# Kernel optimization log

Hardware: AMD Instinct MI355X
Metric: run time of the kernel (lower is better)

## Reference

```python
import jax, jax.numpy as jnp
import numpy as np

EPS = 1e-10      # normalizer eps from the torch module
IN_EPS = 1e-5    # torch InstanceNorm2d default eps
STRIDE = 2
PAD = 1


def _dw_conv_transpose(x, W):
    """Depthwise ConvTranspose2d applied for every output channel at once.

    x: [B, Cin, H, W]
    W: [Cin, Cout, kh, kw]  (W[:, i] is sub_convs[i].weight of shape [Cin, 1, kh, kw])
    returns: [B, Cin, Cout, H', W'] where channel (c, i) = convT of x[:, c] with W[c, i].
    """
    Cin, Cout, kh, kw = W.shape
    # Transposed conv == dilated conv with spatially flipped kernel,
    # lhs_dilation = stride, padding = k - 1 - pad (output_padding = 0).
    rhs = jnp.flip(W, axis=(-2, -1)).reshape(Cin * Cout, 1, kh, kw)
    pad_h = (kh - 1 - PAD, kh - 1 - PAD)
    pad_w = (kw - 1 - PAD, kw - 1 - PAD)
    out = jax.lax.conv_general_dilated(
        x, rhs,
        window_strides=(1, 1),
        padding=(pad_h, pad_w),
        lhs_dilation=(STRIDE, STRIDE),
        dimension_numbers=('NCHW', 'OIHW', 'NCHW'),
        feature_group_count=Cin,
    )  # [B, Cin*Cout, H', W'], group-major: group c -> channels c*Cout:(c+1)*Cout
    B = x.shape[0]
    return out.reshape(B, Cin, Cout, out.shape[2], out.shape[3])


def setup_inputs() -> dict:
    key = jax.random.key(0)
    k1, k2, k3 = jax.random.split(key, 3)
    B, Cin, Cout, H, Wd, K = 2, 64, 64, 48, 48, 4
    x = jax.random.normal(k1, (B, Cin, H, Wd), dtype=jnp.float32)
    # Positive-leaning weights keep the normalizer (convT of ones) away from zero.
    W = 0.05 + 0.1 * jax.random.uniform(k2, (Cin, Cout, K, K), dtype=jnp.float32)
    bias = 0.02 * jax.random.normal(k3, (Cout,), dtype=jnp.float32)
    return {"x": x, "W": W, "bias": bias}


def reference(x, W, bias):
    # numerator: depthwise convT of the input for every (in_ch, out_ch) pair
    num = _dw_conv_transpose(x, W)                       # [B, Cin, Cout, H', W']
    # normalizer: same convT applied to ones (batch-independent -> batch of 1)
    den = _dw_conv_transpose(jnp.ones_like(x[:1]), W) + EPS  # [1, Cin, Cout, H', W']
    out = jnp.sum(num / den, axis=1) + bias[None, :, None, None]  # [B, Cout, H', W']
    # InstanceNorm2d (no affine, biased variance) over spatial dims per (b, c)
    mean = jnp.mean(out, axis=(2, 3), keepdims=True)
    var = jnp.var(out, axis=(2, 3), keepdims=True)
    return (out - mean) / jnp.sqrt(var + IN_EPS)
```

## Files before the change

### kernel.cpp

```cpp
#include <hip/hip_runtime.h>

#define BB    2
#define CIN   64
#define NI    64
#define HIN   48
#define WIN   48
#define HO    96
#define WO    96
#define EPSN  1e-10f
#define IN_EPS 1e-5f
#define IMG   (HO*WO)
#define NIMG  (BB*NI)
#define PH    50
#define PW    52
#define XPN   (BB*CIN*PH*PW)

__global__ __launch_bounds__(256) void pad_kernel(const float* __restrict__ x,
                                                  float* __restrict__ xpad) {
    const int slice = blockIdx.x >> 1, half = blockIdx.x & 1;
    const float* xs = x + (size_t)slice * (HIN * WIN);
    float* xd = xpad + (size_t)slice * (PH * PW) + half * 25 * PW;
    for (int e = threadIdx.x; e < 25 * PW; e += 256) {
        const int rp = e / PW, pc = e - rp * PW;
        const int h = half * 25 + rp - 1, w = pc - 1;
        float v = 0.f;
        if ((unsigned)h < HIN && (unsigned)w < WIN) v = xs[h * WIN + w];
        xd[e] = v;
    }
}

template <int CS>
__global__ __launch_bounds__(256) void conv_kernel(
        const float* __restrict__ xpad, const float* __restrict__ Wt,
        float* __restrict__ part) {
    constexpr int NC = CIN / CS;
    const int bi = blockIdx.x, s = blockIdx.y;
    const int b = bi >> 6, i = bi & 63, c0 = s * NC;
    const int tid = threadIdx.x;
    const int ty = tid >> 4, tx = tid & 15;

    __shared__ __align__(16) float sF[NC * 16];
    __shared__ float sW[NC * 16];
    __shared__ float sR[NC * 16];
    __shared__ float sFix[384];

    for (int e = tid; e < NC * 16; e += 256) {
        const int c = e >> 4, j = e & 15;
        const float* wp = Wt + ((size_t)(c0 + c) * NI + i) * 16;
        sW[e] = wp[j];
        const int py = (j >> 3) & 1, px = (j >> 2) & 1, a = (j >> 1) & 1, bb = j & 1;
        const int kh = py ? (a ? 2 : 0) : (a ? 3 : 1);
        const int kw = px ? (bb ? 2 : 0) : (bb ? 3 : 1);
        const int r0 = py ? 0 : 1, r1 = py ? 2 : 3;
        const int q0 = px ? 0 : 1, q1 = px ? 2 : 3;
        const float den = wp[r0 * 4 + q0] + wp[r0 * 4 + q1]
                        + wp[r1 * 4 + q0] + wp[r1 * 4 + q1];
        sF[e] = wp[kh * 4 + kw] / (den + EPSN);
        const int cy = j >> 2, cx = j & 3;
        const int THn[4] = {1, 2, 2, 1};
        const int THv[4][2] = {{1, 1}, {0, 2}, {1, 3}, {2, 2}};
        float den2 = 0.f;
        for (int aa = 0; aa < THn[cy]; ++aa)
            for (int bb2 = 0; bb2 < THn[cx]; ++bb2)
                den2 += wp[THv[cy][aa] * 4 + THv[cx][bb2]];
        sR[e] = 1.f / (den2 + EPSN);
    }
    __syncthreads();

    float acc[6][6];
#pragma unroll
    for (int r = 0; r < 6; ++r)
#pragma unroll
        for (int j = 0; j < 6; ++j) acc[r][j] = 0.f;

    const float* xb = xpad + ((size_t)b * CIN + c0) * (PH * PW) + (3 * ty) * PW + 3 * tx;

#pragma unroll 2
    for (int c = 0; c < NC; ++c) {
        float g[16];
        const float4* gf = (const float4*)&sF[c * 16];
#pragma unroll
        for (int q = 0; q < 4; ++q) {
            const float4 t = gf[q];
            g[4 * q] = t.x; g[4 * q + 1] = t.y; g[4 * q + 2] = t.z; g[4 * q + 3] = t.w;
        }

        const float* xc = xb + c * (PH * PW);
        float xv[5][5];
#pragma unroll
        for (int rr = 0; rr < 5; ++rr)
#pragma unroll
            for (int cc = 0; cc < 5; ++cc) xv[rr][cc] = xc[rr * PW + cc];

#pragma unroll
        for (int r = 0; r < 6; ++r) {
            const int rhi = (r + 3) >> 1, rlo = rhi - 1, py = r & 1;
#pragma unroll
            for (int j = 0; j < 6; ++j) {
                const int chi = (j + 3) >> 1, clo = chi - 1, px = j & 1;
                const float* gg = &g[py * 8 + px * 4];
                acc[r][j] += xv[rhi][chi] * gg[0] + xv[rhi][clo] * gg[1]
                           + xv[rlo][chi] * gg[2] + xv[rlo][clo] * gg[3];
            }
        }
    }

    const float* xb2 = xpad + ((size_t)b * CIN + c0) * (PH * PW);
    for (int p = tid; p < 380; p += 256) {
        int y, xo;
        if (p < 96)       { y = 0;            xo = p; }
        else if (p < 192) { y = 95;           xo = p - 96; }
        else if (p < 286) { y = p - 192 + 1;  xo = 0; }
        else              { y = p - 286 + 1;  xo = 95; }
        const int hA = (y + 1) >> 1, hB = hA - 1;
        const int khA = (y & 1) ? 0 : 1, khB = khA + 2;
        const int wA = (xo + 1) >> 1, wB = wA - 1;
        const int kwA = (xo & 1) ? 0 : 1, kwB = kwA + 2;
        const int cy = (y == 0) ? 0 : (y == 95) ? 3 : ((y & 1) ? 1 : 2);
        const int cx = (xo == 0) ? 0 : (xo == 95) ? 3 : ((xo & 1) ? 1 : 2);
        const int cls = cy * 4 + cx;
        const int rA = (hA + 1) * PW, rB = (hB + 1) * PW;
        float v = 0.f;
        for (int c = 0; c < NC; ++c) {
            const float* xc = xb2 + c * (PH * PW);
            const float* wc = &sW[c * 16];
            const float num = xc[rA + wA + 1] * wc[khA * 4 + kwA]
                            + xc[rA + wB + 1] * wc[khA * 4 + kwB]
                            + xc[rB + wA + 1] * wc[khB * 4 + kwA]
                            + xc[rB + wB + 1] * wc[khB * 4 + kwB];
            v += num * sR[c * 16 + cls];
        }
        sFix[p] = v;
    }
    __syncthreads();

#pragma unroll
    for (int r = 0; r < 6; ++r)
#pragma unroll
        for (int j = 0; j < 6; ++j) {
            const int y = 6 * ty + r, xo = 6 * tx + j;
            if (y == 0)        acc[r][j] = sFix[xo];
            else if (y == 95)  acc[r][j] = sFix[96 + xo];
            else if (xo == 0)  acc[r][j] = sFix[192 + y - 1];
            else if (xo == 95) acc[r][j] = sFix[286 + y - 1];
        }

    float* pp = part + ((size_t)s * NIMG + bi) * IMG + (6 * ty) * WO + 6 * tx;
#pragma unroll
    for (int r = 0; r < 6; ++r)
#pragma unroll
        for (int jj = 0; jj < 3; ++jj) {
            float2 v;
            v.x = acc[r][2 * jj];
            v.y = acc[r][2 * jj + 1];
            *(float2*)(pp + r * WO + 2 * jj) = v;
        }
}

template <int CS>
__global__ __launch_bounds__(768) void epilogue_kernel(
        const float* __restrict__ part, const float* __restrict__ bias,
        float* __restrict__ out) {
    const int bi = blockIdx.x;
    const int tid = threadIdx.x;
    const float bv = bias[bi & 63];
    const float4* pb = (const float4*)part + (size_t)bi * (IMG / 4);
    const size_t stride4 = (size_t)NIMG * (IMG / 4);

    float4 v[3];
    float s1 = 0.f, s2 = 0.f;
#pragma unroll
    for (int k = 0; k < 3; ++k) {
        const int idx = k * 768 + tid;
        float4 t = pb[idx];
#pragma unroll
        for (int s = 1; s < CS; ++s) {
            const float4 q = pb[s * stride4 + idx];
            t.x += q.x; t.y += q.y; t.z += q.z; t.w += q.w;
        }
        t.x += bv; t.y += bv; t.z += bv; t.w += bv;
        v[k] = t;
        s1 += t.x + t.y + t.z + t.w;
        s2 += t.x * t.x + t.y * t.y + t.z * t.z + t.w * t.w;
    }

    __shared__ float red[24];
    __shared__ float stat[2];
#pragma unroll
    for (int off = 32; off > 0; off >>= 1) {
        s1 += __shfl_down(s1, off, 64);
        s2 += __shfl_down(s2, off, 64);
    }
    const int w = tid >> 6;
    if ((tid & 63) == 0) { red[w] = s1; red[12 + w] = s2; }
    __syncthreads();
    if (tid == 0) {
        float t1 = 0.f, t2 = 0.f;
#pragma unroll
        for (int k = 0; k < 12; ++k) { t1 += red[k]; t2 += red[12 + k]; }
        const float mean = t1 * (1.f / 9216.f);
        const float m2 = t2 * (1.f / 9216.f);
        stat[0] = mean;
        stat[1] = rsqrtf(m2 - mean * mean + IN_EPS);
    }
    __syncthreads();
    const float mean = stat[0], inv = stat[1];

    float4* ob = (float4*)out + (size_t)bi * (IMG / 4);
#pragma unroll
    for (int k = 0; k < 3; ++k) {
        const int idx = k * 768 + tid;
        float4 t = v[k];
        t.x = (t.x - mean) * inv; t.y = (t.y - mean) * inv;
        t.z = (t.z - mean) * inv; t.w = (t.w - mean) * inv;
        ob[idx] = t;
    }
}

extern "C" void kernel_launch(void* const* d_in, const int* in_sizes, int n_in,
                              void* d_out, int out_size, void* d_ws, size_t ws_size,
                              hipStream_t stream) {
    const float* x    = (const float*)d_in[0];
    const float* Wt   = (const float*)d_in[1];
    const float* bias = (const float*)d_in[2];
    float* out = (float*)d_out;
    float* ws  = (float*)d_ws;

    float* xpad = ws;
    pad_kernel<<<BB * CIN * 2, 256, 0, stream>>>(x, xpad);

    const size_t need4 = ((size_t)XPN + (size_t)4 * NIMG * IMG) * 4;
    if (ws_size >= need4) {
        float* part = ws + XPN;
        conv_kernel<4><<<dim3(NIMG, 4), 256, 0, stream>>>(xpad, Wt, part);
        epilogue_kernel<4><<<NIMG, 768, 0, stream>>>(part, bias, out);
    } else {
        conv_kernel<1><<<dim3(NIMG, 1), 256, 0, stream>>>(xpad, Wt, out);
        epilogue_kernel<1><<<NIMG, 768, 0, stream>>>(out, bias, out);
    }
}
```

Before: 96.68 us.

## Recast depthwise convT sum as fp16 MFMA GEMM over channels

Replaces the FP32 scalar conv with a channel-last fp16 layout of x and precomputed fp16 normalized weight matrices, so the per-phase 2x2 taps become MFMA 16x16x32 GEMMs reducing over input channels. The split-channel partial buffers and their summation go away, and border pixels are fixed up in the epilogue instead of the conv. The intent is to move the dominant FLOPs onto matrix cores and cut partial-sum traffic. In exchange it adds fp16 rounding of inputs and weights, and it uses static device globals instead of the workspace.

```diff
diff --git a/kernel.cpp b/kernel.cpp
--- a/kernel.cpp
+++ b/kernel.cpp
@@ -11,172 +11,200 @@
 #define IN_EPS 1e-5f
 #define IMG   (HO*WO)
 #define NIMG  (BB*NI)
-#define PH    50
-#define PW    52
-#define XPN   (BB*CIN*PH*PW)
-
-__global__ __launch_bounds__(256) void pad_kernel(const float* __restrict__ x,
-                                                  float* __restrict__ xpad) {
-    const int slice = blockIdx.x >> 1, half = blockIdx.x & 1;
-    const float* xs = x + (size_t)slice * (HIN * WIN);
-    float* xd = xpad + (size_t)slice * (PH * PW) + half * 25 * PW;
-    for (int e = threadIdx.x; e < 25 * PW; e += 256) {
-        const int rp = e / PW, pc = e - rp * PW;
-        const int h = half * 25 + rp - 1, w = pc - 1;
-        float v = 0.f;
-        if ((unsigned)h < HIN && (unsigned)w < WIN) v = xs[h * WIN + w];
-        xd[e] = v;
-    }
-}
-
-template <int CS>
-__global__ __launch_bounds__(256) void conv_kernel(
-        const float* __restrict__ xpad, const float* __restrict__ Wt,
-        float* __restrict__ part) {
-    constexpr int NC = CIN / CS;
-    const int bi = blockIdx.x, s = blockIdx.y;
-    const int b = bi >> 6, i = bi & 63, c0 = s * NC;
+
+#define XTROW 50
+#define XTSL  (XTROW*XTROW*64)
+
+using half8  = __attribute__((ext_vector_type(8))) _Float16;
+using half2v = __attribute__((ext_vector_type(2))) _Float16;
+using f32x4  = __attribute__((ext_vector_type(4))) float;
+
+__device__ _Float16 g_xt[BB * XTSL];
+__device__ _Float16 g_G[16 * 64 * 64];
+__device__ float    g_out[NIMG * IMG];
+
+__global__ __launch_bounds__(256) void prep_kernel(const float* __restrict__ x,
+                                                   const float* __restrict__ Wt) {
+    const int blk = blockIdx.x;
     const int tid = threadIdx.x;
-    const int ty = tid >> 4, tx = tid & 15;
-
-    __shared__ __align__(16) float sF[NC * 16];
-    __shared__ float sW[NC * 16];
-    __shared__ float sR[NC * 16];
+
+    if (blk < 96) {
+        const int b = blk / 48, h = blk - 48 * b, hp = h + 1;
+        __shared__ float sT[64][49];
+        for (int e = tid; e < 64 * 12; e += 256) {
+            const int c = e / 12, w4 = e - 12 * c;
+            const float4 t = *(const float4*)(x + ((size_t)(b * 64 + c) * 48 + h) * 48 + 4 * w4);
+            sT[c][4 * w4]     = t.x;
+            sT[c][4 * w4 + 1] = t.y;
+            sT[c][4 * w4 + 2] = t.z;
+            sT[c][4 * w4 + 3] = t.w;
+        }
+        __syncthreads();
+        _Float16* xr = g_xt + (size_t)b * XTSL + (size_t)hp * (XTROW * 64);
+        for (int e = tid; e < XTROW * 32; e += 256) {
+            const int wp = e >> 5, cp = e & 31;
+            half2v hv;
+            if (wp == 0 || wp == 49) { hv[0] = (_Float16)0.f; hv[1] = (_Float16)0.f; }
+            else { hv[0] = (_Float16)sT[2 * cp][wp - 1]; hv[1] = (_Float16)sT[2 * cp + 1][wp - 1]; }
+            *(half2v*)(xr + wp * 64 + 2 * cp) = hv;
+        }
+        return;
+    }
+    if (blk < 100) {
+        const int z = blk - 96;
+        const int b = z >> 1, hp = (z & 1) ? 49 : 0;
+        _Float16* xr = g_xt + (size_t)b * XTSL + (size_t)hp * (XTROW * 64);
+        half2v hz; hz[0] = (_Float16)0.f; hz[1] = (_Float16)0.f;
+        for (int e = tid; e < XTROW * 32; e += 256)
+            *(half2v*)(xr + (e >> 5) * 64 + 2 * (e & 31)) = hz;
+        return;
+    }
+    const int combo = blk - 100;
+    const int py = combo >> 3, px = (combo >> 2) & 1, a = (combo >> 1) & 1, bb = combo & 1;
+    const int kh = 2 * a + 1 - py, kw = 2 * bb + 1 - px;
+    for (int e = tid; e < 4096; e += 256) {
+        const int i = e >> 6, c = e & 63;
+        const float* wp = Wt + ((size_t)c * NI + i) * 16;
+        float den = 0.f;
+#pragma unroll
+        for (int a2 = 0; a2 < 2; ++a2)
+#pragma unroll
+            for (int b2 = 0; b2 < 2; ++b2)
+                den += wp[(2 * a2 + 1 - py) * 4 + (2 * b2 + 1 - px)];
+        g_G[combo * 4096 + e] = (_Float16)(wp[kh * 4 + kw] / (den + EPSN));
+    }
+}
+
+__global__ __launch_bounds__(64) void gemm_kernel() {
+    const int blk = blockIdx.x;
+    const int t0 = blk & 1;
+    int rest = blk >> 1;
+    const int n0 = (rest % 3) * 16; rest /= 3;
+    const int r = rest % 48;
+    const int b = rest / 48;
+    const int i0 = 32 * t0;
+    const int lane = threadIdx.x;
+    const int il = lane & 15, q = lane >> 4;
+
+    f32x4 acc[4][2];
+#pragma unroll
+    for (int p = 0; p < 4; ++p)
+#pragma unroll
+        for (int n = 0; n < 2; ++n) { acc[p][n][0] = 0.f; acc[p][n][1] = 0.f; acc[p][n][2] = 0.f; acc[p][n][3] = 0.f; }
+
+    const _Float16* xbase = g_xt + (size_t)b * XTSL
+                          + ((size_t)(r + 1) * XTROW + (n0 + il + 1)) * 64 + q * 8;
+    const _Float16* gbase = g_G + (i0 + il) * 64 + q * 8;
+
+#pragma unroll
+    for (int khalf = 0; khalf < 2; ++khalf) {
+        const int ko = khalf * 32;
+        half8 A[3][3];
+#pragma unroll
+        for (int dr = 0; dr < 3; ++dr)
+#pragma unroll
+            for (int dc = 0; dc < 3; ++dc)
+                A[dr][dc] = *(const half8*)(xbase + (dr - 1) * (XTROW * 64) + (dc - 1) * 64 + ko);
+
+#pragma unroll
+        for (int combo = 0; combo < 16; ++combo) {
+            const int py = combo >> 3, px = (combo >> 2) & 1;
+            const int a = (combo >> 1) & 1, bb = combo & 1;
+            const int pi = combo >> 2;
+            const half8 B0 = *(const half8*)(gbase + combo * 4096 + ko);
+            const half8 B1 = *(const half8*)(gbase + combo * 4096 + 1024 + ko);
+            const half8 Af = A[py - a + 1][px - bb + 1];
+            acc[pi][0] = __builtin_amdgcn_mfma_f32_16x16x32_f16(Af, B0, acc[pi][0], 0, 0, 0);
+            acc[pi][1] = __builtin_amdgcn_mfma_f32_16x16x32_f16(Af, B1, acc[pi][1], 0, 0, 0);
+        }
+    }
+
+#pragma unroll
+    for (int pi = 0; pi < 4; ++pi) {
+        const int py = pi >> 1, px = pi & 1;
+        const int y = 2 * r + py;
+#pragma unroll
+        for (int nt = 0; nt < 2; ++nt) {
+            float* ob = g_out + (size_t)(b * 64 + i0 + 16 * nt + il) * IMG
+                      + y * WO + 2 * n0 + 8 * q + px;
+#pragma unroll
+            for (int reg = 0; reg < 4; ++reg)
+                ob[2 * reg] = acc[pi][nt][reg];
+        }
+    }
+}
+
+__global__ __launch_bounds__(256) void epilogue_kernel(
+        const float* __restrict__ Wt, const float* __restrict__ bias,
+        float* __restrict__ out) {
+    const int bi = blockIdx.x;
+    const int b = bi >> 6, i = bi & 63;
+    const int tid = threadIdx.x;
+
+    __shared__ float sWb[16 * 4 * 64];
     __shared__ float sFix[384];
-
-    for (int e = tid; e < NC * 16; e += 256) {
-        const int c = e >> 4, j = e & 15;
-        const float* wp = Wt + ((size_t)(c0 + c) * NI + i) * 16;
-        sW[e] = wp[j];
-        const int py = (j >> 3) & 1, px = (j >> 2) & 1, a = (j >> 1) & 1, bb = j & 1;
-        const int kh = py ? (a ? 2 : 0) : (a ? 3 : 1);
-        const int kw = px ? (bb ? 2 : 0) : (bb ? 3 : 1);
-        const int r0 = py ? 0 : 1, r1 = py ? 2 : 3;
-        const int q0 = px ? 0 : 1, q1 = px ? 2 : 3;
-        const float den = wp[r0 * 4 + q0] + wp[r0 * 4 + q1]
-                        + wp[r1 * 4 + q0] + wp[r1 * 4 + q1];
-        sF[e] = wp[kh * 4 + kw] / (den + EPSN);
-        const int cy = j >> 2, cx = j & 3;
+    __shared__ float sRed[10];
+
+    for (int e = tid; e < 4096; e += 256) {
+        const int cls = e >> 8, t = (e >> 6) & 3, c = e & 63;
+        const int cy = cls >> 2, cx = cls & 3;
+        const float* wp = Wt + ((size_t)c * NI + i) * 16;
         const int THn[4] = {1, 2, 2, 1};
         const int THv[4][2] = {{1, 1}, {0, 2}, {1, 3}, {2, 2}};
-        float den2 = 0.f;
+        float den = 0.f;
         for (int aa = 0; aa < THn[cy]; ++aa)
-            for (int bb2 = 0; bb2 < THn[cx]; ++bb2)
-                den2 += wp[THv[cy][aa] * 4 + THv[cx][bb2]];
-        sR[e] = 1.f / (den2 + EPSN);
-    }
-    __syncthreads();
-
-    float acc[6][6];
-#pragma unroll
-    for (int r = 0; r < 6; ++r)
-#pragma unroll
-        for (int j = 0; j < 6; ++j) acc[r][j] = 0.f;
-
-    const float* xb = xpad + ((size_t)b * CIN + c0) * (PH * PW) + (3 * ty) * PW + 3 * tx;
-
-#pragma unroll 2
-    for (int c = 0; c < NC; ++c) {
-        float g[16];
-        const float4* gf = (const float4*)&sF[c * 16];
-#pragma unroll
-        for (int q = 0; q < 4; ++q) {
-            const float4 t = gf[q];
-            g[4 * q] = t.x; g[4 * q + 1] = t.y; g[4 * q + 2] = t.z; g[4 * q + 3] = t.w;
-        }
-
-        const float* xc = xb + c * (PH * PW);
-        float xv[5][5];
-#pragma unroll
-        for (int rr = 0; rr < 5; ++rr)
-#pragma unroll
-            for (int cc = 0; cc < 5; ++cc) xv[rr][cc] = xc[rr * PW + cc];
-
-#pragma unroll
-        for (int r = 0; r < 6; ++r) {
-            const int rhi = (r + 3) >> 1, rlo = rhi - 1, py = r & 1;
-#pragma unroll
-            for (int j = 0; j < 6; ++j) {
-                const int chi = (j + 3) >> 1, clo = chi - 1, px = j & 1;
-                const float* gg = &g[py * 8 + px * 4];
-                acc[r][j] += xv[rhi][chi] * gg[0] + xv[rhi][clo] * gg[1]
-                           + xv[rlo][chi] * gg[2] + xv[rlo][clo] * gg[3];
-            }
-        }
-    }
-
-    const float* xb2 = xpad + ((size_t)b * CIN + c0) * (PH * PW);
-    for (int p = tid; p < 380; p += 256) {
+            for (int bb = 0; bb < THn[cx]; ++bb)
+                den += wp[THv[cy][aa] * 4 + THv[cx][bb]];
+        const int khA = (cy & 1) ? 0 : 1, kwA = (cx & 1) ? 0 : 1;
+        const int kh = (t >> 1) ? khA + 2 : khA;
+        const int kw = (t & 1) ? kwA + 2 : kwA;
+        sWb[e] = wp[kh * 4 + kw] / (den + EPSN);
+    }
+    __syncthreads();
+
+    const _Float16* xb = g_xt + (size_t)b * XTSL;
+#pragma unroll
+    for (int k = 0; k < 2; ++k) {
+        const int p = tid + 256 * k;
+        if (p >= 380) break;
         int y, xo;
         if (p < 96)       { y = 0;            xo = p; }
         else if (p < 192) { y = 95;           xo = p - 96; }
         else if (p < 286) { y = p - 192 + 1;  xo = 0; }
         else              { y = p - 286 + 1;  xo = 95; }
-        const int hA = (y + 1) >> 1, hB = hA - 1;
-        const int khA = (y & 1) ? 0 : 1, khB = khA + 2;
-        const int wA = (xo + 1) >> 1, wB = wA - 1;
-        const int kwA = (xo & 1) ? 0 : 1, kwB = kwA + 2;
+        const int hpA = ((y + 1) >> 1) + 1, hpB = hpA - 1;
+        const int wpA = ((xo + 1) >> 1) + 1, wpB = wpA - 1;
         const int cy = (y == 0) ? 0 : (y == 95) ? 3 : ((y & 1) ? 1 : 2);
         const int cx = (xo == 0) ? 0 : (xo == 95) ? 3 : ((xo & 1) ? 1 : 2);
-        const int cls = cy * 4 + cx;
-        const int rA = (hA + 1) * PW, rB = (hB + 1) * PW;
-        float v = 0.f;
-        for (int c = 0; c < NC; ++c) {
-            const float* xc = xb2 + c * (PH * PW);
-            const float* wc = &sW[c * 16];
-            const float num = xc[rA + wA + 1] * wc[khA * 4 + kwA]
-                            + xc[rA + wB + 1] * wc[khA * 4 + kwB]
-                            + xc[rB + wA + 1] * wc[khB * 4 + kwA]
-                            + xc[rB + wB + 1] * wc[khB * 4 + kwB];
-            v += num * sR[c * 16 + cls];
-        }
-        sFix[p] = v;
-    }
-    __syncthreads();
-
-#pragma unroll
-    for (int r = 0; r < 6; ++r)
-#pragma unroll
-        for (int j = 0; j < 6; ++j) {
-            const int y = 6 * ty + r, xo = 6 * tx + j;
-            if (y == 0)        acc[r][j] = sFix[xo];
-            else if (y == 95)  acc[r][j] = sFix[96 + xo];
-            else if (xo == 0)  acc[r][j] = sFix[192 + y - 1];
-            else if (xo == 95) acc[r][j] = sFix[286 + y - 1];
-        }
-
-    float* pp = part + ((size_t)s * NIMG + bi) * IMG + (6 * ty) * WO + 6 * tx;
-#pragma unroll
-    for (int r = 0; r < 6; ++r)
-#pragma unroll
-        for (int jj = 0; jj < 3; ++jj) {
-            float2 v;
-            v.x = acc[r][2 * jj];
-            v.y = acc[r][2 * jj + 1];
-            *(float2*)(pp + r * WO + 2 * jj) = v;
-        }
-}
-
-template <int CS>
-__global__ __launch_bounds__(768) void epilogue_kernel(
-        const float* __restrict__ part, const float* __restrict__ bias,
-        float* __restrict__ out) {
-    const int bi = blockIdx.x;
-    const int tid = threadIdx.x;
-    const float bv = bias[bi & 63];
-    const float4* pb = (const float4*)part + (size_t)bi * (IMG / 4);
-    const size_t stride4 = (size_t)NIMG * (IMG / 4);
-
-    float4 v[3];
+        const float* w0 = &sWb[(cy * 4 + cx) * 256];
+        const _Float16* pAA = xb + (hpA * XTROW + wpA) * 64;
+        const _Float16* pAB = xb + (hpA * XTROW + wpB) * 64;
+        const _Float16* pBA = xb + (hpB * XTROW + wpA) * 64;
+        const _Float16* pBB = xb + (hpB * XTROW + wpB) * 64;
+        float acc = 0.f;
+#pragma unroll 8
+        for (int c = 0; c < 64; ++c)
+            acc += (float)pAA[c] * w0[c]       + (float)pAB[c] * w0[64 + c]
+                 + (float)pBA[c] * w0[128 + c] + (float)pBB[c] * w0[192 + c];
+        sFix[p] = acc;
+    }
+    __syncthreads();
+
+    const float bv = bias[i];
+    const float4* gb = (const float4*)(g_out + (size_t)bi * IMG);
+    float4 v[9];
     float s1 = 0.f, s2 = 0.f;
 #pragma unroll
-    for (int k = 0; k < 3; ++k) {
-        const int idx = k * 768 + tid;
-        float4 t = pb[idx];
-#pragma unroll
-        for (int s = 1; s < CS; ++s) {
-            const float4 q = pb[s * stride4 + idx];
-            t.x += q.x; t.y += q.y; t.z += q.z; t.w += q.w;
+    for (int k = 0; k < 9; ++k) {
+        const int idx = k * 256 + tid;
+        float4 t = gb[idx];
+        const int p = 4 * idx;
+        const int y = p / 96, xq = p - 96 * y;
+        if (y == 0)       { t.x = sFix[xq]; t.y = sFix[xq + 1]; t.z = sFix[xq + 2]; t.w = sFix[xq + 3]; }
+        else if (y == 95) { t.x = sFix[96 + xq]; t.y = sFix[97 + xq]; t.z = sFix[98 + xq]; t.w = sFix[99 + xq]; }
+        else {
+            if (xq == 0)  t.x = sFix[192 + y - 1];
+            if (xq == 92) t.w = sFix[286 + y - 1];
         }
         t.x += bv; t.y += bv; t.z += bv; t.w += bv;
         v[k] = t;
@@ -184,36 +212,32 @@
         s2 += t.x * t.x + t.y * t.y + t.z * t.z + t.w * t.w;
     }
 
-    __shared__ float red[24];
-    __shared__ float stat[2];
 #pragma unroll
     for (int off = 32; off > 0; off >>= 1) {
         s1 += __shfl_down(s1, off, 64);
         s2 += __shfl_down(s2, off, 64);
     }
     const int w = tid >> 6;
-    if ((tid & 63) == 0) { red[w] = s1; red[12 + w] = s2; }
+    if ((tid & 63) == 0) { sRed[w] = s1; sRed[4 + w] = s2; }
     __syncthreads();
     if (tid == 0) {
-        float t1 = 0.f, t2 = 0.f;
-#pragma unroll
-        for (int k = 0; k < 12; ++k) { t1 += red[k]; t2 += red[12 + k]; }
+        const float t1 = sRed[0] + sRed[1] + sRed[2] + sRed[3];
+        const float t2 = sRed[4] + sRed[5] + sRed[6] + sRed[7];
         const float mean = t1 * (1.f / 9216.f);
         const float m2 = t2 * (1.f / 9216.f);
-        stat[0] = mean;
-        stat[1] = rsqrtf(m2 - mean * mean + IN_EPS);
-    }
-    __syncthreads();
-    const float mean = stat[0], inv = stat[1];
+        sRed[8] = mean;
+        sRed[9] = rsqrtf(m2 - mean * mean + IN_EPS);
+    }
+    __syncthreads();
+    const float mean = sRed[8], inv = sRed[9];
 
     float4* ob = (float4*)out + (size_t)bi * (IMG / 4);
 #pragma unroll
-    for (int k = 0; k < 3; ++k) {
-        const int idx = k * 768 + tid;
+    for (int k = 0; k < 9; ++k) {
         float4 t = v[k];
         t.x = (t.x - mean) * inv; t.y = (t.y - mean) * inv;
         t.z = (t.z - mean) * inv; t.w = (t.w - mean) * inv;
-        ob[idx] = t;
+        ob[k * 256 + tid] = t;
     }
 }
 
@@ -224,18 +248,9 @@
     const float* Wt   = (const float*)d_in[1];
     const float* bias = (const float*)d_in[2];
     float* out = (float*)d_out;
-    float* ws  = (float*)d_ws;
-
-    float* xpad = ws;
-    pad_kernel<<<BB * CIN * 2, 256, 0, stream>>>(x, xpad);
-
-    const size_t need4 = ((size_t)XPN + (size_t)4 * NIMG * IMG) * 4;
-    if (ws_size >= need4) {
-        float* part = ws + XPN;
-        conv_kernel<4><<<dim3(NIMG, 4), 256, 0, stream>>>(xpad, Wt, part);
-        epilogue_kernel<4><<<NIMG, 768, 0, stream>>>(part, bias, out);
-    } else {
-        conv_kernel<1><<<dim3(NIMG, 1), 256, 0, stream>>>(xpad, Wt, out);
-        epilogue_kernel<1><<<NIMG, 768, 0, stream>>>(out, bias, out);
-    }
-}
+    (void)d_ws; (void)ws_size;
+
+    prep_kernel<<<116, 256, 0, stream>>>(x, Wt);
+    gemm_kernel<<<576, 64, 0, stream>>>();
+    epilogue_kernel<<<128, 256, 0, stream>>>(Wt, bias, out);
+}
```

Measured after the change: 101.0 us. 4.5% more time.
